# Kernel tuning notes

Measured on AMD Instinct MI355X. Metric: run time of the kernel, lower is better.

## Reference

```python
import jax, jax.numpy as jnp
import numpy as np

HIDDEN = 4096
N_HEADS = 32
N_KV_HEADS = 8
HEAD_DIM = HIDDEN // N_HEADS  # 128
GROUPS = N_HEADS // N_KV_HEADS  # 4
ATTN_MULT = 0.08838834764831845  # 1/sqrt(head_dim)
MAX_ATTN_VAL = 30.0
NEG_INF = -1e30


def setup_inputs() -> dict:
    key = jax.random.key(0)
    ks = jax.random.split(key, 5)
    B, S = 2, 2048
    hidden_states = jax.random.normal(ks[0], (B, S, HIDDEN), dtype=jnp.float32)
    scale = 1.0 / np.sqrt(HIDDEN)
    Wq = jax.random.normal(ks[1], (HIDDEN, N_HEADS * HEAD_DIM), dtype=jnp.float32) * scale
    Wk = jax.random.normal(ks[2], (HIDDEN, N_KV_HEADS * HEAD_DIM), dtype=jnp.float32) * scale
    Wv = jax.random.normal(ks[3], (HIDDEN, N_KV_HEADS * HEAD_DIM), dtype=jnp.float32) * scale
    Wo = jax.random.normal(ks[4], (N_HEADS * HEAD_DIM, HIDDEN), dtype=jnp.float32) * scale
    return {"hidden_states": hidden_states, "Wq": Wq, "Wk": Wk, "Wv": Wv, "Wo": Wo}


def reference(hidden_states, Wq, Wk, Wv, Wo):
    B, S, _ = hidden_states.shape
    # projections
    q = (hidden_states @ Wq).reshape(B, S, N_HEADS, HEAD_DIM).transpose(0, 2, 1, 3)      # bhsd
    k = (hidden_states @ Wk).reshape(B, S, N_KV_HEADS, HEAD_DIM).transpose(0, 2, 1, 3)   # bksd
    v = (hidden_states @ Wv).reshape(B, S, N_KV_HEADS, HEAD_DIM).transpose(0, 2, 1, 3)
    # GQA: expand kv heads to query heads
    k = jnp.repeat(k, GROUPS, axis=1)  # [B, N_HEADS, S, D]
    v = jnp.repeat(v, GROUPS, axis=1)
    # scaled scores with Grok-style tanh soft-cap
    scores = jnp.einsum('bhqd,bhkd->bhqk', q, k) * ATTN_MULT
    scores = MAX_ATTN_VAL * jnp.tanh(scores / MAX_ATTN_VAL)
    # causal mask
    causal = jnp.tril(jnp.ones((S, S), dtype=bool))
    scores = jnp.where(causal[None, None], scores, NEG_INF)
    probs = jax.nn.softmax(scores.astype(jnp.float32), axis=-1).astype(v.dtype)
    out = jnp.einsum('bhqk,bhkd->bhqd', probs, v)          # [B, H, S, D]
    out = out.transpose(0, 2, 1, 3).reshape(B, S, N_HEADS * HEAD_DIM)
    return out @ Wo
```

## Files before the change

### kernel.cpp

```cpp
#include <hip/hip_runtime.h>
#include <hip/hip_bf16.h>
#include <type_traits>
#include <utility>
#include <cmath>

#define HIDDEN 4096
#define NHEADS 32
#define NKV 8
#define HD 128
#define BB 2
#define SS 2048
#define NTOK (BB*SS)
#define ATTN_MULT 0.08838834764831845f

using bf16x8 = __attribute__((ext_vector_type(8))) short;
using f32x4  = __attribute__((ext_vector_type(4))) float;

using gas = __attribute__((address_space(1))) const void;
using las = __attribute__((address_space(3))) void;

__device__ __forceinline__ unsigned short f2bf(float f){
  unsigned int u = __builtin_bit_cast(unsigned int, f);
  u += 0x7fffu + ((u >> 16) & 1u);
  return (unsigned short)(u >> 16);
}
__device__ __forceinline__ unsigned int cvtpk(float lo, float hi){
  unsigned int r;
  asm("v_cvt_pk_bf16_f32 %0, %1, %2" : "=v"(r) : "v"(lo), "v"(hi));
  return r;
}
__device__ __forceinline__ float exp2_hw(float x){
  float r;
  asm("v_exp_f32 %0, %1" : "=v"(r) : "v"(x));
  return r;
}

#define LOG2E 1.4426950408889634f
#define C1L  (-5.3433149e-4f)
#define C2L  (2.3748069e-7f)
#define B30L (-43.280851227f)

__global__ void cvt_f32_bf16_k(const float* __restrict__ in, unsigned short* __restrict__ out, int n8){
  int i = blockIdx.x * blockDim.x + threadIdx.x;
  if (i >= n8) return;
  const float4* p = (const float4*)in + (size_t)i * 2;
  float4 a = p[0], b = p[1];
  bf16x8 o;
  o[0]=f2bf(a.x); o[1]=f2bf(a.y); o[2]=f2bf(a.z); o[3]=f2bf(a.w);
  o[4]=f2bf(b.x); o[5]=f2bf(b.y); o[6]=f2bf(b.z); o[7]=f2bf(b.w);
  ((bf16x8*)out)[i] = o;
}

__global__ void transpose_cvt_k(const float* __restrict__ W, unsigned short* __restrict__ WT, int K, int N){
  __shared__ float tile[32][33];
  int n0 = blockIdx.x * 32, k0 = blockIdx.y * 32;
  int tx = threadIdx.x, ty = threadIdx.y;
  #pragma unroll
  for (int i = 0; i < 4; ++i)
    tile[ty*4+i][tx] = W[(size_t)(k0 + ty*4 + i) * N + n0 + tx];
  __syncthreads();
  #pragma unroll
  for (int i = 0; i < 4; ++i)
    WT[(size_t)(n0 + ty*4 + i) * K + k0 + tx] = f2bf(tile[tx][ty*4+i]);
}

__global__ void transpose_v_k(const unsigned short* __restrict__ in, unsigned short* __restrict__ out){
  __shared__ unsigned short tile[32][33];
  int c0 = blockIdx.x * 32, r0 = blockIdx.y * 32;
  int tx = threadIdx.x, ty = threadIdx.y;
  #pragma unroll
  for (int i = 0; i < 4; ++i)
    tile[ty*4+i][tx] = in[(size_t)(r0 + ty*4 + i) * 2048 + 1024 + c0 + tx];
  __syncthreads();
  #pragma unroll
  for (int i = 0; i < 4; ++i){
    int c = c0 + ty*4 + i, r = r0 + tx;
    out[((size_t)((r >> 11) * 1024 + c)) * 2048 + (r & 2047)] = tile[tx][ty*4+i];
  }
}

template<typename OutT>
__global__ __launch_bounds__(256, 3)
void gemm_bt_k(const unsigned short* __restrict__ A,
               const unsigned short* __restrict__ BT,
               OutT* __restrict__ C, int M, int N, int K){
  __shared__ __align__(16) unsigned short As[128*32];
  __shared__ __align__(16) unsigned short Bs[128*32];
  const int m0 = blockIdx.y * 128, n0 = blockIdx.x * 128;
  const int tid = threadIdx.x, w = tid >> 6, lane = tid & 63;
  const int wr = w >> 1, wc = w & 1;
  const int lrow = lane & 15, lk = (lane >> 4) * 8;
  const int arow = lane >> 2, acol = (lane & 3) * 8;

  f32x4 acc[4][4] = {};

  for (int k0 = 0; k0 < K; k0 += 32){
    #pragma unroll
    for (int i = 0; i < 2; ++i){
      int chunk = w*2 + i;
      const unsigned short* ga = A  + (size_t)(m0 + chunk*16 + arow) * K + k0 + acol;
      const unsigned short* gb = BT + (size_t)(n0 + chunk*16 + arow) * K + k0 + acol;
      __builtin_amdgcn_global_load_lds((gas*)ga, (las*)(As + chunk*512), 16, 0, 0);
      __builtin_amdgcn_global_load_lds((gas*)gb, (las*)(Bs + chunk*512), 16, 0, 0);
    }
    __syncthreads();
    bf16x8 af[4], bfr[4];
    #pragma unroll
    for (int m = 0; m < 4; ++m) af[m]  = *(const bf16x8*)&As[(wr*64 + m*16 + lrow)*32 + lk];
    #pragma unroll
    for (int n = 0; n < 4; ++n) bfr[n] = *(const bf16x8*)&Bs[(wc*64 + n*16 + lrow)*32 + lk];
    #pragma unroll
    for (int m = 0; m < 4; ++m)
      #pragma unroll
      for (int n = 0; n < 4; ++n)
        acc[m][n] = __builtin_amdgcn_mfma_f32_16x16x32_bf16(af[m], bfr[n], acc[m][n], 0, 0, 0);
    __syncthreads();
  }

  const int crow = (lane >> 4) * 4, ccol = lane & 15;
  #pragma unroll
  for (int m = 0; m < 4; ++m)
    #pragma unroll
    for (int n = 0; n < 4; ++n){
      size_t base = (size_t)(m0 + wr*64 + m*16 + crow) * N + n0 + wc*64 + n*16 + ccol;
      #pragma unroll
      for (int r = 0; r < 4; ++r){
        float v = acc[m][n][r];
        if constexpr (std::is_same<OutT, unsigned short>::value) C[base + (size_t)r*N] = f2bf(v);
        else                                                     C[base + (size_t)r*N] = v;
      }
    }
}

#define GBAR() asm volatile("s_barrier" ::: "memory")

template<typename OutT>
__global__ __launch_bounds__(512, 2)
void gemm8_k(const unsigned short* __restrict__ A,
             const unsigned short* __restrict__ BT,
             OutT* __restrict__ C, int M, int N, int K, float scale){
  __shared__ __align__(16) unsigned short As[2][256*64];
  __shared__ __align__(16) unsigned short Bs[2][256*64];

  const int nbx = N >> 8;
  const int id = blockIdx.x + blockIdx.y * nbx;
  const int nwg = nbx * (M >> 8);
  const int swz = (id & 7) * (nwg >> 3) + (id >> 3);
  const int m0 = (swz / nbx) << 8, n0 = (swz % nbx) << 8;

  const int tid = threadIdx.x, w = tid >> 6, lane = tid & 63;
  const int wm = w >> 2, wn = w & 3;
  const int lrow = lane & 15, lhi = lane >> 4;
  const int l3 = lane >> 3, k8l = lane & 7;
  const int NT = K >> 6;

  f32x4 acc[8][4] = {};
  bf16x8 bf[4][2];

  auto stageB = [&](int t, int s, int half){
    #pragma unroll
    for (int j = 0; j < 2; ++j){
      int row0 = half*128 + j*64 + w*8;
      int row = row0 + l3;
      const unsigned short* g = BT + (size_t)(n0 + row) * K + t*64 + ((k8l ^ (row & 7)) << 3);
      __builtin_amdgcn_global_load_lds((gas*)g, (las*)(&Bs[s][0] + row0*64), 16, 0, 0);
    }
  };
  auto stageA = [&](int t, int s, int g2){
    #pragma unroll
    for (int j = 0; j < 2; ++j){
      int g = g2 + j;
      int row0 = ((w >= 4) ? 128 : 0) + g*32 + (w & 3)*8;
      int row = row0 + l3;
      const unsigned short* ga = A + (size_t)(m0 + row) * K + t*64 + ((k8l ^ (row & 7)) << 3);
      __builtin_amdgcn_global_load_lds((gas*)ga, (las*)(&As[s][0] + row0*64), 16, 0, 0);
    }
  };

  stageB(0, 0, 0); stageB(0, 0, 1); stageA(0, 0, 0); stageA(0, 0, 2);
  asm volatile("s_waitcnt vmcnt(0)");
  GBAR();

  #pragma unroll 1
  for (int t = 0; t < NT; ++t){
    const int cur = t & 1, nxt = cur ^ 1;
    const bool pre = (t + 1 < NT);

    if (pre){ stageB(t+1, nxt, 0); stageB(t+1, nxt, 1); stageA(t+1, nxt, 0); stageA(t+1, nxt, 2); }

    #pragma unroll
    for (int nf = 0; nf < 4; ++nf)
      #pragma unroll
      for (int kk = 0; kk < 2; ++kk){
        int row = wn*64 + nf*16 + lrow;
        int c8 = (kk*4 + lhi) ^ (row & 7);
        bf[nf][kk] = *(const bf16x8*)&Bs[cur][row*64 + c8*8];
      }
    bf16x8 af[4][2][2];
    #pragma unroll
    for (int P = 0; P < 2; ++P)
      #pragma unroll
      for (int mi = 0; mi < 2; ++mi)
        #pragma unroll
        for (int kk = 0; kk < 2; ++kk){
          int row = wm*128 + P*32 + mi*16 + lrow;
          int c8 = (kk*4 + lhi) ^ (row & 7);
          af[P][mi][kk] = *(const bf16x8*)&As[cur][row*64 + c8*8];
        }

    __builtin_amdgcn_s_setprio(1);
    #pragma unroll
    for (int P = 0; P < 4; ++P){
      if (P < 2){
        const int Q = P + 2;
        #pragma unroll
        for (int mi = 0; mi < 2; ++mi)
          #pragma unroll
          for (int kk = 0; kk < 2; ++kk){
            int row = wm*128 + Q*32 + mi*16 + lrow;
            int c8 = (kk*4 + lhi) ^ (row & 7);
            af[Q][mi][kk] = *(const bf16x8*)&As[cur][row*64 + c8*8];
          }
      }
      #pragma unroll
      for (int mi = 0; mi < 2; ++mi)
        #pragma unroll
        for (int nf = 0; nf < 4; ++nf)
          #pragma unroll
          for (int kk = 0; kk < 2; ++kk)
            acc[P*2+mi][nf] = __builtin_amdgcn_mfma_f32_16x16x32_bf16(
                af[P][mi][kk], bf[nf][kk], acc[P*2+mi][nf], 0, 0, 0);
    }
    __builtin_amdgcn_s_setprio(0);

    if (pre) asm volatile("s_waitcnt vmcnt(0)");
    GBAR();
  }

  #pragma unroll
  for (int mf = 0; mf < 8; ++mf)
    #pragma unroll
    for (int nf = 0; nf < 4; ++nf){
      size_t base = (size_t)(m0 + wm*128 + mf*16 + lhi*4) * N + n0 + wn*64 + nf*16 + lrow;
      #pragma unroll
      for (int r = 0; r < 4; ++r){
        float v = acc[mf][nf][r] * scale;
        if constexpr (std::is_same<OutT, unsigned short>::value) C[base + (size_t)r*N] = f2bf(v);
        else                                                     C[base + (size_t)r*N] = v;
      }
    }
}

__global__ __launch_bounds__(512, 2)
void attn_k(const unsigned short* __restrict__ Q,
            const unsigned short* __restrict__ KVp,
            const unsigned short* __restrict__ VTp,
            unsigned short* __restrict__ ctx){
  __shared__ __align__(16) unsigned short Ks[2][64*128];
  __shared__ __align__(16) unsigned short Vt[2][128*64];
  __shared__ __align__(16) unsigned short Ps[8][1024];

  const int Wb = blockIdx.x;
  const int xcd = Wb & 7, sI = Wb >> 3;
  const int gsub = sI >> 4;
  const int inner = sI & 15;
  const int hsH = inner >> 2;
  const int fi = inner & 3;
  const int group = xcd*2 + gsub;
  const int b = group >> 3, kvh = group & 7;
  const int h = kvh*4 + hsH;

  const int tid = threadIdx.x, w = tid >> 6, lane = tid & 63;
  const int lrow = lane & 15, lhi = lane >> 4;
  const int xorv = (lrow & 3) << 4;

  const unsigned short* Kbh  = KVp + (size_t)b * SS * 2048 + kvh * HD;
  const unsigned short* VTbh = VTp + ((size_t)b * 1024 + kvh * HD) * SS;

  auto STAGE = [&](int db, int t){
    #pragma unroll
    for (int it = 0; it < 2; ++it){
      int cbase = it*512 + w*64;
      int c = cbase + lane;
      int kkv = c >> 4, kc = c & 15;
      const unsigned short* gk = Kbh + (size_t)(t*64 + kkv) * 2048 + ((kc ^ (kkv & 7)) << 3);
      __builtin_amdgcn_global_load_lds((gas*)gk, (las*)(&Ks[db][0] + cbase*8), 16, 0, 0);
      int vd = c >> 3, vc = c & 7;
      const unsigned short* gv = VTbh + (size_t)vd * SS + t*64 + ((vc ^ ((vd ^ (vd >> 3)) & 7)) << 3);
      __builtin_amdgcn_global_load_lds((gas*)gv, (las*)(&Vt[db][0] + cbase*8), 16, 0, 0);
    }
  };

  #pragma unroll 1
  for (int ph = 0; ph < 2; ++ph){
    const int strip = ph ? (7 - fi) : fi;
    const int qwb = strip*256 + w*32;
    const int nt = strip*4 + 4;

    bf16x8 qf[2][4];
    {
      const unsigned short* qb = Q + (size_t)(b*SS + qwb + lrow) * 4096 + h*HD + lhi*8;
      #pragma unroll
      for (int qg = 0; qg < 2; ++qg)
        #pragma unroll
        for (int ks = 0; ks < 4; ++ks)
          qf[qg][ks] = *(const bf16x8*)(qb + (size_t)qg*16*4096 + ks*32);
    }

    f32x4 o[8][2] = {};
    float psum[2] = {0.f, 0.f};

    STAGE(0, 0);
    __syncthreads();

    for (int t = 0; t < nt; ++t){
      const int db = t & 1;
      if (t + 1 < nt) STAGE(db ^ 1, t + 1);

      if (t*64 <= qwb + 31){
        const char* Kc = (const char*)&Ks[db][0];
        const char* Vc = (const char*)&Vt[db][0];
        char* Pw = (char*)&Ps[w][0];

        auto body = [&](auto DIAG){
          #pragma unroll
          for (int hh = 0; hh < 2; ++hh){
            f32x4 sacc[2][2];
            #pragma unroll
            for (int cc = 0; cc < 2; ++cc){
              const int row = (hh*2 + cc)*16 + lrow;
              bf16x8 kf[4];
              #pragma unroll
              for (int ks = 0; ks < 4; ++ks){
                int kbyte = (row*256 + (ks*32 + lhi*8)*2) ^ ((row & 7) << 4);
                kf[ks] = *(const bf16x8*)(Kc + kbyte);
              }
              f32x4 s0 = {0.f,0.f,0.f,0.f}, s1 = {0.f,0.f,0.f,0.f};
              __builtin_amdgcn_s_setprio(1);
              #pragma unroll
              for (int ks = 0; ks < 4; ++ks){
                s0 = __builtin_amdgcn_mfma_f32_16x16x32_bf16(kf[ks], qf[0][ks], s0, 0, 0, 0);
                s1 = __builtin_amdgcn_mfma_f32_16x16x32_bf16(kf[ks], qf[1][ks], s1, 0, 0, 0);
              }
              __builtin_amdgcn_s_setprio(0);
              sacc[0][cc] = s0; sacc[1][cc] = s1;
            }

            #pragma unroll
            for (int qg = 0; qg < 2; ++qg){
              const int qglob = qwb + qg*16 + lrow;
              #pragma unroll
              for (int cc = 0; cc < 2; ++cc){
                float pv[4];
                #pragma unroll
                for (int r = 0; r < 4; ++r){
                  float s = __builtin_amdgcn_fmed3f(sacc[qg][cc][r], -25.f, 25.f);
                  float s2 = s*s, s4 = s2*s2;
                  float wv = __builtin_fmaf(s2, C1L, LOG2E);
                  wv = __builtin_fmaf(s4, C2L, wv);
                  float p = exp2_hw(__builtin_fmaf(s, wv, B30L));
                  if constexpr (decltype(DIAG)::value){
                    int kvg = t*64 + (hh*2 + cc)*16 + lhi*4 + r;
                    p = (kvg <= qglob) ? p : 0.f;
                  }
                  psum[qg] += p;
                  pv[r] = p;
                }
                uint2 pk;
                pk.x = cvtpk(pv[0], pv[1]);
                pk.y = cvtpk(pv[2], pv[3]);
                *(uint2*)(Pw + qg*1024 + lrow*64 + ((cc*32 + lhi*8) ^ xorv)) = pk;
              }
            }

            bf16x8 pf0 = *(const bf16x8*)(Pw +        lrow*64 + ((lhi*16) ^ xorv));
            bf16x8 pf1 = *(const bf16x8*)(Pw + 1024 + lrow*64 + ((lhi*16) ^ xorv));
            __builtin_amdgcn_s_setprio(1);
            #pragma unroll
            for (int df = 0; df < 8; ++df){
              int d = df*16 + lrow;
              int vbyte = (d*128 + (hh*32 + lhi*8)*2) ^ (((d ^ (d >> 3)) & 7) << 4);
              bf16x8 vf = *(const bf16x8*)(Vc + vbyte);
              o[df][0] = __builtin_amdgcn_mfma_f32_16x16x32_bf16(vf, pf0, o[df][0], 0, 0, 0);
              o[df][1] = __builtin_amdgcn_mfma_f32_16x16x32_bf16(vf, pf1, o[df][1], 0, 0, 0);
            }
            __builtin_amdgcn_s_setprio(0);
          }
        };
        if (t == (qwb >> 6)) body(std::true_type{});
        else                 body(std::false_type{});
      }
      __syncthreads();
    }

    #pragma unroll
    for (int qg = 0; qg < 2; ++qg){
      float sum = psum[qg];
      sum += __shfl_xor(sum, 16);
      sum += __shfl_xor(sum, 32);
      float inv = 1.f / sum;
      unsigned short* base = ctx + (size_t)(b*SS + qwb + qg*16 + lrow) * 4096 + h*HD + lhi*4;
      #pragma unroll
      for (int df = 0; df < 8; ++df){
        uint2 pk;
        pk.x = cvtpk(o[df][qg][0] * inv, o[df][qg][1] * inv);
        pk.y = cvtpk(o[df][qg][2] * inv, o[df][qg][3] * inv);
        *(uint2*)(base + df*16) = pk;
      }
    }
    __syncthreads();
  }
}

#define O_HSB   ((size_t)0)
#define O_WQT   ((size_t)33554432)
#define O_WKT   ((size_t)67108864)
#define O_WVT   ((size_t)75497472)
#define O_WOT   ((size_t)83886080)
#define O_Q     ((size_t)117440512)
#define O_KV    ((size_t)150994944)
#define O_CTX   ((size_t)167772160)
#define WS_NEED ((size_t)201326592)

extern "C" void kernel_launch(void* const* d_in, const int* in_sizes, int n_in,
                              void* d_out, int out_size, void* d_ws, size_t ws_size,
                              hipStream_t stream){
  if (ws_size < WS_NEED) return;
  const float* hs = (const float*)d_in[0];
  const float* Wq = (const float*)d_in[1];
  const float* Wk = (const float*)d_in[2];
  const float* Wv = (const float*)d_in[3];
  const float* Wo = (const float*)d_in[4];
  char* ws = (char*)d_ws;
  unsigned short* hsb = (unsigned short*)(ws + O_HSB);
  unsigned short* WqT = (unsigned short*)(ws + O_WQT);
  unsigned short* WkT = (unsigned short*)(ws + O_WKT);
  unsigned short* WvT = (unsigned short*)(ws + O_WVT);
  unsigned short* WoT = (unsigned short*)(ws + O_WOT);
  unsigned short* Qb  = (unsigned short*)(ws + O_Q);
  unsigned short* KVb = (unsigned short*)(ws + O_KV);
  unsigned short* ctxb= (unsigned short*)(ws + O_CTX);
  unsigned short* VTb = (unsigned short*)(ws + O_WQT);

  cvt_f32_bf16_k<<<dim3((NTOK*HIDDEN/8)/256), dim3(256), 0, stream>>>(hs, hsb, NTOK*HIDDEN/8);
  transpose_cvt_k<<<dim3(128,128), dim3(32,8), 0, stream>>>(Wq, WqT, 4096, 4096);
  transpose_cvt_k<<<dim3(32,128),  dim3(32,8), 0, stream>>>(Wk, WkT, 4096, 1024);
  transpose_cvt_k<<<dim3(32,128),  dim3(32,8), 0, stream>>>(Wv, WvT, 4096, 1024);
  transpose_cvt_k<<<dim3(128,128), dim3(32,8), 0, stream>>>(Wo, WoT, 4096, 4096);
  gemm8_k<unsigned short><<<dim3(16,16), dim3(512), 0, stream>>>(hsb, WqT, Qb, 4096, 4096, 4096, ATTN_MULT);
  gemm_bt_k<unsigned short><<<dim3(16,32), dim3(256), 0, stream>>>(hsb, WkT, KVb, 4096, 2048, 4096);
  transpose_v_k<<<dim3(32,128), dim3(32,8), 0, stream>>>(KVb, VTb);
  attn_k<<<dim3(256), dim3(512), 0, stream>>>(Qb, KVb, VTb, ctxb);
  gemm8_k<float><<<dim3(16,16), dim3(512), 0, stream>>>(ctxb, WoT, (float*)d_out, 4096, 4096, 4096, 1.0f);
}
```

Before: 531.8 us.

## Split GEMM k-step into two phases with partial vmcnt waits and extra barriers

Restructures the double-buffered GEMM main loop into two half-steps. Each half loads A fragments from LDS, issues part of the next tile's global-to-LDS loads, waits with a partial vmcnt count instead of draining all loads, syncs, and then runs half of the MFMAs. This aims to overlap global loads with compute more finely and to cut register pressure by keeping only two A fragment groups live. In exchange it adds a second barrier per iteration, and the vmcnt counts must match the issue order exactly or the kernel reads stale LDS data.

```diff
diff --git a/kernel.cpp b/kernel.cpp
--- a/kernel.cpp
+++ b/kernel.cpp
@@ -177,16 +177,15 @@
     }
   };
 
-  stageB(0, 0, 0); stageB(0, 0, 1); stageA(0, 0, 0); stageA(0, 0, 2);
-  asm volatile("s_waitcnt vmcnt(0)");
+  stageA(0, 0, 0); stageB(0, 0, 0); stageB(0, 0, 1); stageA(0, 0, 2);
+  asm volatile("s_waitcnt vmcnt(2)");
   GBAR();
 
   #pragma unroll 1
   for (int t = 0; t < NT; ++t){
     const int cur = t & 1, nxt = cur ^ 1;
     const bool pre = (t + 1 < NT);
-
-    if (pre){ stageB(t+1, nxt, 0); stageB(t+1, nxt, 1); stageA(t+1, nxt, 0); stageA(t+1, nxt, 2); }
+    bf16x8 af[2][2][2];
 
     #pragma unroll
     for (int nf = 0; nf < 4; ++nf)
@@ -196,7 +195,6 @@
         int c8 = (kk*4 + lhi) ^ (row & 7);
         bf[nf][kk] = *(const bf16x8*)&Bs[cur][row*64 + c8*8];
       }
-    bf16x8 af[4][2][2];
     #pragma unroll
     for (int P = 0; P < 2; ++P)
       #pragma unroll
@@ -207,21 +205,16 @@
           int c8 = (kk*4 + lhi) ^ (row & 7);
           af[P][mi][kk] = *(const bf16x8*)&As[cur][row*64 + c8*8];
         }
-
+    if (pre){
+      stageA(t+1, nxt, 0); stageB(t+1, nxt, 0); stageB(t+1, nxt, 1);
+      asm volatile("s_waitcnt vmcnt(6)");
+    } else {
+      asm volatile("s_waitcnt vmcnt(0)");
+    }
+    GBAR();
     __builtin_amdgcn_s_setprio(1);
     #pragma unroll
-    for (int P = 0; P < 4; ++P){
-      if (P < 2){
-        const int Q = P + 2;
-        #pragma unroll
-        for (int mi = 0; mi < 2; ++mi)
-          #pragma unroll
-          for (int kk = 0; kk < 2; ++kk){
-            int row = wm*128 + Q*32 + mi*16 + lrow;
-            int c8 = (kk*4 + lhi) ^ (row & 7);
-            af[Q][mi][kk] = *(const bf16x8*)&As[cur][row*64 + c8*8];
-          }
-      }
+    for (int P = 0; P < 2; ++P)
       #pragma unroll
       for (int mi = 0; mi < 2; ++mi)
         #pragma unroll
@@ -230,11 +223,35 @@
           for (int kk = 0; kk < 2; ++kk)
             acc[P*2+mi][nf] = __builtin_amdgcn_mfma_f32_16x16x32_bf16(
                 af[P][mi][kk], bf[nf][kk], acc[P*2+mi][nf], 0, 0, 0);
-    }
     __builtin_amdgcn_s_setprio(0);
 
-    if (pre) asm volatile("s_waitcnt vmcnt(0)");
+    #pragma unroll
+    for (int P = 0; P < 2; ++P)
+      #pragma unroll
+      for (int mi = 0; mi < 2; ++mi)
+        #pragma unroll
+        for (int kk = 0; kk < 2; ++kk){
+          int row = wm*128 + (P+2)*32 + mi*16 + lrow;
+          int c8 = (kk*4 + lhi) ^ (row & 7);
+          af[P][mi][kk] = *(const bf16x8*)&As[cur][row*64 + c8*8];
+        }
+    if (pre){
+      stageA(t+1, nxt, 2);
+      asm volatile("s_waitcnt vmcnt(2)");
+    }
     GBAR();
+    __builtin_amdgcn_s_setprio(1);
+    #pragma unroll
+    for (int P = 0; P < 2; ++P)
+      #pragma unroll
+      for (int mi = 0; mi < 2; ++mi)
+        #pragma unroll
+        for (int nf = 0; nf < 4; ++nf)
+          #pragma unroll
+          for (int kk = 0; kk < 2; ++kk)
+            acc[(P+2)*2+mi][nf] = __builtin_amdgcn_mfma_f32_16x16x32_bf16(
+                af[P][mi][kk], bf[nf][kk], acc[(P+2)*2+mi][nf], 0, 0, 0);
+    __builtin_amdgcn_s_setprio(0);
   }
 
   #pragma unroll
```

Measured after the change: 500.3 us (median of 2 runs). 1.06x faster.

## Switch GEMM to 3-stage LDS ring with K-tile of 32 and one barrier

Applied to the files above, without the earlier changes.

The 256x256 GEMM kernel now uses a triple-buffered LDS ring with a K-step of 32 instead of a double buffer with a K-step of 64. It keeps one tile load in flight across each barrier through a partial vmcnt wait, with a single barrier per iteration. The LDS swizzle changes to match the narrower rows, and A and B staging are merged into one loop. This is meant to hide global-to-LDS latency better and cut the time spent at the barrier. In exchange there are twice as many iterations, and each one does half the MFMA work, so per-iteration barrier and address overhead grows relative to compute.

```diff
diff --git a/kernel.cpp b/kernel.cpp
--- a/kernel.cpp
+++ b/kernel.cpp
@@ -139,8 +139,8 @@
 void gemm8_k(const unsigned short* __restrict__ A,
              const unsigned short* __restrict__ BT,
              OutT* __restrict__ C, int M, int N, int K, float scale){
-  __shared__ __align__(16) unsigned short As[2][256*64];
-  __shared__ __align__(16) unsigned short Bs[2][256*64];
+  __shared__ __align__(16) unsigned short As[3][256*32];
+  __shared__ __align__(16) unsigned short Bs[3][256*32];
 
   const int nbx = N >> 8;
   const int id = blockIdx.x + blockIdx.y * nbx;
@@ -151,90 +151,59 @@
   const int tid = threadIdx.x, w = tid >> 6, lane = tid & 63;
   const int wm = w >> 2, wn = w & 3;
   const int lrow = lane & 15, lhi = lane >> 4;
-  const int l3 = lane >> 3, k8l = lane & 7;
-  const int NT = K >> 6;
+  const int NT = K >> 5;
 
   f32x4 acc[8][4] = {};
-  bf16x8 bf[4][2];
-
-  auto stageB = [&](int t, int s, int half){
+
+  auto STG = [&](int t, int s){
     #pragma unroll
     for (int j = 0; j < 2; ++j){
-      int row0 = half*128 + j*64 + w*8;
-      int row = row0 + l3;
-      const unsigned short* g = BT + (size_t)(n0 + row) * K + t*64 + ((k8l ^ (row & 7)) << 3);
-      __builtin_amdgcn_global_load_lds((gas*)g, (las*)(&Bs[s][0] + row0*64), 16, 0, 0);
+      int c = j*512 + tid;
+      int row = c >> 2, kc = c & 3;
+      int ksw = (kc ^ ((row >> 1) & 3)) << 3;
+      int cbase = (j*512 + w*64) * 8;
+      const unsigned short* ga = A  + (size_t)(m0 + row) * K + t*32 + ksw;
+      __builtin_amdgcn_global_load_lds((gas*)ga, (las*)(&As[s][0] + cbase), 16, 0, 0);
+      const unsigned short* gb = BT + (size_t)(n0 + row) * K + t*32 + ksw;
+      __builtin_amdgcn_global_load_lds((gas*)gb, (las*)(&Bs[s][0] + cbase), 16, 0, 0);
     }
   };
-  auto stageA = [&](int t, int s, int g2){
-    #pragma unroll
-    for (int j = 0; j < 2; ++j){
-      int g = g2 + j;
-      int row0 = ((w >= 4) ? 128 : 0) + g*32 + (w & 3)*8;
-      int row = row0 + l3;
-      const unsigned short* ga = A + (size_t)(m0 + row) * K + t*64 + ((k8l ^ (row & 7)) << 3);
-      __builtin_amdgcn_global_load_lds((gas*)ga, (las*)(&As[s][0] + row0*64), 16, 0, 0);
-    }
-  };
-
-  stageB(0, 0, 0); stageB(0, 0, 1); stageA(0, 0, 0); stageA(0, 0, 2);
-  asm volatile("s_waitcnt vmcnt(0)");
-  GBAR();
+
+  STG(0, 0);
+  int cur = 0, nxt = 1;
 
   #pragma unroll 1
   for (int t = 0; t < NT; ++t){
-    const int cur = t & 1, nxt = cur ^ 1;
-    const bool pre = (t + 1 < NT);
-
-    if (pre){ stageB(t+1, nxt, 0); stageB(t+1, nxt, 1); stageA(t+1, nxt, 0); stageA(t+1, nxt, 2); }
-
-    #pragma unroll
-    for (int nf = 0; nf < 4; ++nf)
-      #pragma unroll
-      for (int kk = 0; kk < 2; ++kk){
-        int row = wn*64 + nf*16 + lrow;
-        int c8 = (kk*4 + lhi) ^ (row & 7);
-        bf[nf][kk] = *(const bf16x8*)&Bs[cur][row*64 + c8*8];
-      }
-    bf16x8 af[4][2][2];
-    #pragma unroll
-    for (int P = 0; P < 2; ++P)
-      #pragma unroll
-      for (int mi = 0; mi < 2; ++mi)
-        #pragma unroll
-        for (int kk = 0; kk < 2; ++kk){
-          int row = wm*128 + P*32 + mi*16 + lrow;
-          int c8 = (kk*4 + lhi) ^ (row & 7);
-          af[P][mi][kk] = *(const bf16x8*)&As[cur][row*64 + c8*8];
-        }
-
+    if (t + 1 < NT){
+      STG(t + 1, nxt);
+      asm volatile("s_waitcnt vmcnt(4)");
+    } else {
+      asm volatile("s_waitcnt vmcnt(0)");
+    }
+    GBAR();
+
+    bf16x8 bfr[4], af[8];
+    #pragma unroll
+    for (int nf = 0; nf < 4; ++nf){
+      int row = wn*64 + nf*16 + lrow;
+      int ch = lhi ^ ((row >> 1) & 3);
+      bfr[nf] = *(const bf16x8*)&Bs[cur][row*32 + ch*8];
+    }
+    #pragma unroll
+    for (int mf = 0; mf < 8; ++mf){
+      int row = wm*128 + mf*16 + lrow;
+      int ch = lhi ^ ((row >> 1) & 3);
+      af[mf] = *(const bf16x8*)&As[cur][row*32 + ch*8];
+    }
     __builtin_amdgcn_s_setprio(1);
     #pragma unroll
-    for (int P = 0; P < 4; ++P){
-      if (P < 2){
-        const int Q = P + 2;
-        #pragma unroll
-        for (int mi = 0; mi < 2; ++mi)
-          #pragma unroll
-          for (int kk = 0; kk < 2; ++kk){
-            int row = wm*128 + Q*32 + mi*16 + lrow;
-            int c8 = (kk*4 + lhi) ^ (row & 7);
-            af[Q][mi][kk] = *(const bf16x8*)&As[cur][row*64 + c8*8];
-          }
-      }
-      #pragma unroll
-      for (int mi = 0; mi < 2; ++mi)
-        #pragma unroll
-        for (int nf = 0; nf < 4; ++nf)
-          #pragma unroll
-          for (int kk = 0; kk < 2; ++kk)
-            acc[P*2+mi][nf] = __builtin_amdgcn_mfma_f32_16x16x32_bf16(
-                af[P][mi][kk], bf[nf][kk], acc[P*2+mi][nf], 0, 0, 0);
-    }
+    for (int mf = 0; mf < 8; ++mf)
+      #pragma unroll
+      for (int nf = 0; nf < 4; ++nf)
+        acc[mf][nf] = __builtin_amdgcn_mfma_f32_16x16x32_bf16(af[mf], bfr[nf], acc[mf][nf], 0, 0, 0);
     __builtin_amdgcn_s_setprio(0);
 
-    if (pre) asm volatile("s_waitcnt vmcnt(0)");
-    GBAR();
+    cur = nxt; ++nxt; if (nxt == 3) nxt = 0;
   }
 
   #pragma unroll
```

Measured after the change: 523.6 us. No clear change (-1.5%).
